# Performance work log

Hardware: AMD Instinct MI355X
Metric: run time of the kernel (lower is better)

## Reference

```python
import jax, jax.numpy as jnp
import numpy as np

NPOINT = 2048
RADIUS = 0.4
NSAMPLE = 32
BN_EPS = 1e-5


def setup_inputs() -> dict:
    key = jax.random.key(0)
    ks = jax.random.split(key, 6)
    B, N, C = 8, 8192, 64
    xyz = jax.random.normal(ks[0], (B, N, 3), jnp.float32)
    points = jax.random.normal(ks[1], (B, N, C), jnp.float32)
    W1 = jax.random.normal(ks[2], (3 + C, 64), jnp.float32) * 0.1
    W2 = jax.random.normal(ks[3], (64, 64), jnp.float32) * 0.1
    W3 = jax.random.normal(ks[4], (64, 128), jnp.float32) * 0.1
    return dict(
        xyz=xyz, points=points,
        W1=W1, g1=jnp.ones(64), b1=jnp.zeros(64),
        W2=W2, g2=jnp.ones(64), b2=jnp.zeros(64),
        W3=W3, g3=jnp.ones(128), b3=jnp.zeros(128),
    )


def _furthest_point_sample(xyz, npoint):
    # xyz: (B, N, 3) -> (B, npoint) int32. Sequential max-min scan, batched.
    B, N, _ = xyz.shape

    def step(carry, _):
        dists, last = carry
        p = jnp.take_along_axis(xyz, last[:, None, None], axis=1)  # (B,1,3)
        d2 = jnp.sum((xyz - p) ** 2, axis=-1)                       # (B,N)
        dists = jnp.minimum(dists, d2)
        nxt = jnp.argmax(dists, axis=-1).astype(jnp.int32)
        return (dists, nxt), nxt

    init = (jnp.full((B, N), 1e10, xyz.dtype), jnp.zeros((B,), jnp.int32))
    _, idx = jax.lax.scan(step, init, None, length=npoint - 1)      # (npoint-1, B)
    idx = jnp.concatenate([jnp.zeros((1, B), jnp.int32), idx], axis=0)
    return idx.T                                                    # (B, npoint)


def _ball_query(xyz, new_xyz, radius, nsample):
    # For each centroid take the first nsample point indices (in original order)
    # within `radius`; pad with the first found index (CUDA ball_query semantics).
    B, N, _ = xyz.shape
    d2 = jnp.sum((new_xyz[:, :, None, :] - xyz[:, None, :, :]) ** 2, axis=-1)  # (B,S,N)
    mask = d2 < radius * radius
    key = jnp.where(mask, jnp.arange(N, dtype=jnp.int32), N)
    srt = jnp.sort(key, axis=-1)[..., :nsample]                     # (B,S,K)
    first = srt[..., :1]
    first = jnp.where(first == N, 0, first)                         # empty ball -> index 0
    return jnp.where(srt == N, first, srt)


def _gather(pts, idx):
    # pts: (B,N,D), idx: (B,...) -> (B,...,D)
    return jax.vmap(lambda p, i: p[i])(pts, idx)


def reference(xyz, points, W1, g1, b1, W2, g2, b2, W3, g3, b3):
    fps_idx = _furthest_point_sample(xyz, NPOINT)                   # (B,S)
    new_xyz = _gather(xyz, fps_idx)                                 # (B,S,3)
    idx = _ball_query(xyz, new_xyz, RADIUS, NSAMPLE)                # (B,S,K)
    grouped_xyz = _gather(xyz, idx) - new_xyz[:, :, None, :]        # (B,S,K,3)
    grouped_pts = _gather(points, idx)                              # (B,S,K,C)
    feats = jnp.concatenate([grouped_xyz, grouped_pts], axis=-1)    # (B,S,K,3+C)
    for W, g, b in ((W1, g1, b1), (W2, g2, b2), (W3, g3, b3)):
        feats = feats @ W                                           # 1x1 conv
        m = feats.mean(axis=(0, 1, 2))
        v = feats.var(axis=(0, 1, 2))                               # biased, torch BN train mode
        feats = g * (feats - m) * jax.lax.rsqrt(v + BN_EPS) + b
        feats = jax.nn.relu(feats)
    new_points = feats.max(axis=2)                                  # max over nsample -> (B,S,mlp[-1])
    return new_xyz, new_points
```

## Files before the change

### kernel.cpp

```cpp
#include <hip/hip_runtime.h>

constexpr int B_ = 8, N_ = 8192, NPOINT_ = 2048, NSAMPLE_ = 32;
constexpr int M_ROWS = B_ * NPOINT_ * NSAMPLE_;
constexpr int NGROUP = B_ * NPOINT_;
constexpr size_t OFF_NXF   = 0;
constexpr size_t OFF_IDX   = 196608;
constexpr size_t OFF_WF    = 1245184;
constexpr size_t OFF_GB    = 1311488;
constexpr size_t OFF_STATS = 1313536;
constexpr size_t OFF_NP    = 1315584;
constexpr size_t OFF_FLAG  = 1317632;
constexpr size_t OFF_MAXB  = 2097152;

__device__ __forceinline__ float bf2f(unsigned short u) {
  union { unsigned u; float f; } x; x.u = ((unsigned)u) << 16; return x.f;
}
__device__ __forceinline__ float lo16f(unsigned u) {
  union { unsigned u; float f; } x; x.u = u << 16; return x.f;
}
__device__ __forceinline__ float hi16f(unsigned u) {
  union { unsigned u; float f; } x; x.u = u & 0xffff0000u; return x.f;
}
__device__ __forceinline__ unsigned short f2bf(float f) {
  union { float f; unsigned u; } x; x.f = f;
  unsigned u = x.u + 0x7FFFu + ((x.u >> 16) & 1u);
  return (unsigned short)(u >> 16);
}
__device__ __forceinline__ unsigned f2u(float f) {
  union { float f; unsigned u; } x; x.f = f; return x.u;
}
__device__ __forceinline__ void unpack8(uint4 u, float* x) {
  x[0] = bf2f((unsigned short)(u.x & 0xffffu)); x[1] = bf2f((unsigned short)(u.x >> 16));
  x[2] = bf2f((unsigned short)(u.y & 0xffffu)); x[3] = bf2f((unsigned short)(u.y >> 16));
  x[4] = bf2f((unsigned short)(u.z & 0xffffu)); x[5] = bf2f((unsigned short)(u.z >> 16));
  x[6] = bf2f((unsigned short)(u.w & 0xffffu)); x[7] = bf2f((unsigned short)(u.w >> 16));
}
__device__ __forceinline__ float ldf(const void* p, size_t i, bool bf) {
  return bf ? bf2f(((const unsigned short*)p)[i]) : ((const float*)p)[i];
}
__device__ __forceinline__ void stf(void* p, size_t i, bool bf, float v) {
  if (bf) ((unsigned short*)p)[i] = f2bf(v);
  else    ((float*)p)[i] = v;
}

extern "C" __global__ void detect_kernel(const unsigned short* __restrict__ xyz,
                                         int* __restrict__ flag) {
  if (threadIdx.x == 0 && blockIdx.x == 0) {
    int sane = 0;
    for (int k = 0; k < 32; ++k) {
      int e = (xyz[2 * k] >> 7) & 0xff;
      if (e >= 90 && e <= 140) ++sane;
    }
    *flag = (sane >= 24) ? 1 : 0;
  }
}

extern "C" __global__ void prep_kernel(
    const void* W1, const void* W2, const void* W3,
    const void* g1, const void* b1, const void* g2, const void* b2,
    const void* g3, const void* b3,
    float* __restrict__ wf, float* __restrict__ gb, const int* __restrict__ flag) {
  const bool bf = (*flag != 0);
  int i = blockIdx.x * 256 + threadIdx.x;
  if (i < 4288)       wf[i] = ldf(W1, i, bf);
  else if (i < 8384)  wf[i] = ldf(W2, i - 4288, bf);
  else if (i < 16576) wf[i] = ldf(W3, i - 8384, bf);
  else if (i < 17088) {
    int k = i - 16576; float v;
    if (k < 64)       v = ldf(g1, k, bf);
    else if (k < 128) v = ldf(b1, k - 64, bf);
    else if (k < 192) v = ldf(g2, k - 128, bf);
    else if (k < 256) v = ldf(b2, k - 192, bf);
    else if (k < 384) v = ldf(g3, k - 256, bf);
    else              v = ldf(b3, k - 384, bf);
    gb[k] = v;
  }
}

template <bool BF>
__device__ __forceinline__ void fps_body(
    const void* xyz, void* out, float* __restrict__ nxf,
    unsigned short* sxyz, unsigned long long* slots) {
#pragma clang fp contract(off)
  const int b = blockIdx.x;
  const int t = threadIdx.x;
  const int lane = t & 63;
  const size_t base = (size_t)b * N_ * 3;
  float px[8], py[8], pz[8], d[8];
  if (BF) {
    const uint4* xp = (const uint4*)((const unsigned short*)xyz + base) + t * 3;
    uint4* sp = (uint4*)sxyz + t * 3;
    unsigned cc[12];
#pragma unroll
    for (int m = 0; m < 3; ++m) {
      uint4 u = xp[m];
      sp[m] = u;
      cc[4*m+0] = u.x; cc[4*m+1] = u.y; cc[4*m+2] = u.z; cc[4*m+3] = u.w;
    }
#pragma unroll
    for (int k = 0; k < 8; ++k) {
      if ((k & 1) == 0) {
        unsigned ra = cc[(3*k) >> 1], rb = cc[((3*k) >> 1) + 1];
        px[k] = lo16f(ra); py[k] = hi16f(ra); pz[k] = lo16f(rb);
      } else {
        unsigned ra = cc[(3*k - 1) >> 1], rb = cc[(3*k + 1) >> 1];
        px[k] = hi16f(ra); py[k] = lo16f(rb); pz[k] = hi16f(rb);
      }
    }
  } else {
#pragma unroll
    for (int k = 0; k < 8; ++k) {
      int i = t * 8 + k;
      px[k] = ((const float*)xyz)[base + i*3 + 0];
      py[k] = ((const float*)xyz)[base + i*3 + 1];
      pz[k] = ((const float*)xyz)[base + i*3 + 2];
    }
  }
#pragma unroll
  for (int k = 0; k < 8; ++k) d[k] = 1e10f;
  if (t < 3) slots[t] = 0ull;
  __syncthreads();
  float s0x=0.f,s0y=0.f,s0z=0.f, s1x=0.f,s1y=0.f,s1z=0.f;
  float p0, p1, p2;
  if (BF) { p0 = bf2f(sxyz[0]); p1 = bf2f(sxyz[1]); p2 = bf2f(sxyz[2]); }
  else {
    p0 = ((const float*)xyz)[base + 0];
    p1 = ((const float*)xyz)[base + 1];
    p2 = ((const float*)xyz)[base + 2];
  }
  if (t == 0) { s0x = p0; s0y = p1; s0z = p2; }
  for (int j = 1; j < NPOINT_; ++j) {
    float bv = -1.0f;
#pragma unroll
    for (int k = 0; k < 8; ++k) {
      float dx = px[k] - p0, dy = py[k] - p1, dz = pz[k] - p2;
      float d2 = (dx*dx + dy*dy) + dz*dz;
      float dn = fminf(d[k], d2);
      d[k] = dn;
      bv = fmaxf(bv, dn);
    }
    float bv0 = bv;
#pragma unroll
    for (int off = 1; off < 64; off <<= 1)
      bv = fmaxf(bv, __shfl_xor(bv, off));
    int bk = 0;
    bool hit = (bv0 == bv);
    if (hit) {
#pragma unroll
      for (int k = 7; k >= 0; --k)
        if (d[k] == bv0) bk = k;
    }
    unsigned long long m = __ballot(hit);
    int sl = (int)__builtin_ctzll(m);
    int pi = __shfl(t * 8 + bk, sl);
    const int ss = j % 3;
    if (lane == 0) {
      unsigned long long key =
          ((unsigned long long)f2u(bv) << 32) | (unsigned)(~pi);
      atomicMax(&slots[ss], key);
    }
    if (t == 0) slots[(ss + 1) % 3] = 0ull;
    __syncthreads();
    unsigned long long key2 = slots[ss];
    int gpi = (int)(~(unsigned)key2);
    if (BF) {
      int wo3 = gpi * 3;
      p0 = bf2f(sxyz[wo3 + 0]); p1 = bf2f(sxyz[wo3 + 1]); p2 = bf2f(sxyz[wo3 + 2]);
    } else {
      size_t wo = base + (size_t)gpi * 3;
      p0 = ((const float*)xyz)[wo + 0];
      p1 = ((const float*)xyz)[wo + 1];
      p2 = ((const float*)xyz)[wo + 2];
    }
    if (t == (j & 1023)) {
      if ((j >> 10) == 0) { s0x = p0; s0y = p1; s0z = p2; }
      else                { s1x = p0; s1y = p1; s1z = p2; }
    }
  }
  const bool bfrt = BF;
#pragma unroll
  for (int s = 0; s < 2; ++s) {
    float cx = (s==0)?s0x:s1x;
    float cy = (s==0)?s0y:s1y;
    float cz = (s==0)?s0z:s1z;
    size_t o = ((size_t)b * NPOINT_ + s * 1024 + t) * 3;
    nxf[o+0] = cx; nxf[o+1] = cy; nxf[o+2] = cz;
    stf(out, o+0, bfrt, cx); stf(out, o+1, bfrt, cy); stf(out, o+2, bfrt, cz);
  }
}

extern "C" __global__ void __launch_bounds__(1024, 4) fps_kernel(
    const void* xyz, void* out, float* __restrict__ nxf,
    const int* __restrict__ flag) {
  __shared__ unsigned short sxyz[N_ * 3];
  __shared__ unsigned long long slots[3];
  if (*flag != 0) fps_body<true>(xyz, out, nxf, sxyz, slots);
  else            fps_body<false>(xyz, out, nxf, sxyz, slots);
}

extern "C" __global__ void __launch_bounds__(256) ballq_kernel(
    const void* xyz, const float* __restrict__ nxf,
    unsigned short* __restrict__ idxout, const int* __restrict__ flag) {
#pragma clang fp contract(off)
  const bool bf = (*flag != 0);
  const int gw = (int)((blockIdx.x * 256 + threadIdx.x) >> 6);
  const int lane = threadIdx.x & 63;
  const int b = gw >> 11;
  const int j = gw & (NPOINT_ - 1);
  const size_t base = (size_t)b * N_ * 3;
  const size_t co = ((size_t)b * NPOINT_ + j) * 3;
  const float c0 = nxf[co], c1 = nxf[co+1], c2 = nxf[co+2];
  unsigned short* out = idxout + (size_t)gw * NSAMPLE_;
  int cnt = 0, first = 0;
  for (int c = 0; c < N_/64 && cnt < NSAMPLE_; ++c) {
    int i = c * 64 + lane;
    float x = ldf(xyz, base + i*3 + 0, bf);
    float y = ldf(xyz, base + i*3 + 1, bf);
    float z = ldf(xyz, base + i*3 + 2, bf);
    float dx = x - c0, dy = y - c1, dz = z - c2;
    float d2 = (dx*dx + dy*dy) + dz*dz;
    unsigned long long m = __ballot(d2 < 0.16f);
    if (lane == 0) {
      while (m && cnt < NSAMPLE_) {
        int bit = __builtin_ctzll(m);
        int pi = c * 64 + bit;
        if (cnt == 0) first = pi;
        out[cnt] = (unsigned short)pi;
        ++cnt;
        m &= (m - 1);
      }
    }
    cnt = __shfl(cnt, 0);
  }
  first = __shfl(first, 0);
  if (lane >= cnt && lane < NSAMPLE_) out[lane] = (unsigned short)first;
}

__device__ __forceinline__ void l1_row(
    const void* xyz, const void* points, const float* __restrict__ nxf,
    const unsigned short* __restrict__ idx, const float* __restrict__ wf,
    int r, bool bf, float* acc) {
  const int b = r >> 16;
  const int j = (r >> 5) & (NPOINT_ - 1);
  const int i = idx[r];
  const size_t pt = (size_t)b * N_ + i;
  const float* cp = nxf + ((size_t)b * NPOINT_ + j) * 3;
  float f0 = ldf(xyz, pt*3 + 0, bf) - cp[0];
  float f1 = ldf(xyz, pt*3 + 1, bf) - cp[1];
  float f2 = ldf(xyz, pt*3 + 2, bf) - cp[2];
#pragma unroll
  for (int c = 0; c < 64; ++c)
    acc[c] = fmaf(f0, wf[c], fmaf(f1, wf[64+c], f2 * wf[128+c]));
  const float* wp = wf + 192;
  if (bf) {
    const uint4* pp = (const uint4*)((const unsigned short*)points + pt * 64);
#pragma unroll
    for (int s = 0; s < 8; ++s) {
      uint4 u = pp[s];
      float x[8]; unpack8(u, x);
#pragma unroll
      for (int kk = 0; kk < 8; ++kk)
#pragma unroll
        for (int c = 0; c < 64; ++c)
          acc[c] = fmaf(x[kk], wp[(s*8+kk)*64 + c], acc[c]);
    }
  } else {
    const float4* pp = (const float4*)((const float*)points + pt * 64);
#pragma unroll
    for (int s = 0; s < 16; ++s) {
      float4 u = pp[s];
      float x[4] = {u.x, u.y, u.z, u.w};
#pragma unroll
      for (int kk = 0; kk < 4; ++kk)
#pragma unroll
        for (int c = 0; c < 64; ++c)
          acc[c] = fmaf(x[kk], wp[(s*4+kk)*64 + c], acc[c]);
    }
  }
}

template <int LDW>
__device__ __forceinline__ void mm64(const float* v, const float* __restrict__ w,
                                     float* acc) {
#pragma unroll
  for (int ch = 0; ch < 64; ++ch)
#pragma unroll
    for (int c = 0; c < 64; ++c)
      acc[c] = fmaf(v[ch], w[ch*LDW + c], acc[c]);
}

__device__ __forceinline__ void bnrelu64(float* v, const float* __restrict__ np0) {
#pragma unroll
  for (int c = 0; c < 64; ++c)
    v[c] = fmaxf(fmaf(v[c], np0[c], np0[64 + c]), 0.f);
}

__device__ __forceinline__ void commit_stats64(float* a, float* __restrict__ stats) {
  float q[64];
#pragma unroll
  for (int c = 0; c < 64; ++c) q[c] = a[c] * a[c];
#pragma unroll
  for (int off = 1; off < 64; off <<= 1)
#pragma unroll
    for (int c = 0; c < 64; ++c) {
      a[c] += __shfl_xor(a[c], off);
      q[c] += __shfl_xor(q[c], off);
    }
  __shared__ float LS[4][64], LQ[4][64];
  const int t = threadIdx.x, w = t >> 6;
  if ((t & 63) == 0) {
#pragma unroll
    for (int c = 0; c < 64; ++c) { LS[w][c] = a[c]; LQ[w][c] = q[c]; }
  }
  __syncthreads();
  if (t < 64) {
    atomicAdd(&stats[t],      LS[0][t] + LS[1][t] + LS[2][t] + LS[3][t]);
    atomicAdd(&stats[64 + t], LQ[0][t] + LQ[1][t] + LQ[2][t] + LQ[3][t]);
  }
}

extern "C" __global__ void __launch_bounds__(256) p1_kernel(
    const void* xyz, const void* points, const float* __restrict__ nxf,
    const unsigned short* __restrict__ idx, const float* __restrict__ wf,
    float* __restrict__ stats, const int* __restrict__ flag) {
  const bool bf = (*flag != 0);
  const int r = blockIdx.x * 256 + threadIdx.x;
  float acc[64];
  l1_row(xyz, points, nxf, idx, wf, r, bf, acc);
  commit_stats64(acc, stats);
}

extern "C" __global__ void __launch_bounds__(256, 2) p2_kernel(
    const void* xyz, const void* points, const float* __restrict__ nxf,
    const unsigned short* __restrict__ idx, const float* __restrict__ wf,
    const float* __restrict__ w2, const float* __restrict__ np1,
    float* __restrict__ stats, const int* __restrict__ flag) {
  const bool bf = (*flag != 0);
  const int r = blockIdx.x * 256 + threadIdx.x;
  float v[64];
  l1_row(xyz, points, nxf, idx, wf, r, bf, v);
  bnrelu64(v, np1);
  float acc[64];
#pragma unroll
  for (int c = 0; c < 64; ++c) acc[c] = 0.f;
  mm64<64>(v, w2, acc);
  commit_stats64(acc, stats);
}

extern "C" __global__ void __launch_bounds__(256, 2) p3_kernel(
    const void* xyz, const void* points, const float* __restrict__ nxf,
    const unsigned short* __restrict__ idx, const float* __restrict__ wf,
    const float* __restrict__ w2, const float* __restrict__ w3,
    const float* __restrict__ np1, const float* __restrict__ np2,
    unsigned short* __restrict__ maxb, float* __restrict__ stats,
    const int* __restrict__ flag) {
  const bool bf = (*flag != 0);
  const int t = threadIdx.x, lane = t & 63, w = t >> 6;
  const int h = __builtin_amdgcn_readfirstlane(w & 1);
  const int g = blockIdx.x * 4 + (w >> 1) * 2 + (lane >> 5);
  const int r = g * 32 + (lane & 31);
  float v[64];
  l1_row(xyz, points, nxf, idx, wf, r, bf, v);
  bnrelu64(v, np1);
  float y2[64];
#pragma unroll
  for (int c = 0; c < 64; ++c) y2[c] = 0.f;
  mm64<64>(v, w2, y2);
  bnrelu64(y2, np2);
  const float* w3h = w3 + h * 64;
  float y3[64];
#pragma unroll
  for (int c = 0; c < 64; ++c) y3[c] = 0.f;
  mm64<128>(y2, w3h, y3);
  float* s = v; float* q = y2;
#pragma unroll
  for (int c = 0; c < 64; ++c) { s[c] = y3[c]; q[c] = y3[c] * y3[c]; }
#pragma unroll
  for (int off = 1; off <= 16; off <<= 1)
#pragma unroll
    for (int c = 0; c < 64; ++c)
      y3[c] = fmaxf(y3[c], __shfl_xor(y3[c], off));
  if ((lane & 31) == 0) {
    unsigned short* mo = maxb + (size_t)g * 128 + h * 64;
#pragma unroll
    for (int c = 0; c < 64; ++c) mo[c] = f2bf(y3[c]);
  }
#pragma unroll
  for (int off = 1; off < 64; off <<= 1)
#pragma unroll
    for (int c = 0; c < 64; ++c) {
      s[c] += __shfl_xor(s[c], off);
      q[c] += __shfl_xor(q[c], off);
    }
  __shared__ float LS[4][64], LQ[4][64];
  if (lane == 0) {
#pragma unroll
    for (int c = 0; c < 64; ++c) { LS[w][c] = s[c]; LQ[w][c] = q[c]; }
  }
  __syncthreads();
  if (t < 128) {
    int hh = t >> 6, cl = t & 63;
    atomicAdd(&stats[t],       LS[hh][cl] + LS[hh+2][cl]);
    atomicAdd(&stats[128 + t], LQ[hh][cl] + LQ[hh+2][cl]);
  }
}

extern "C" __global__ void nparam_kernel(
    const float* __restrict__ stats, const float* __restrict__ g,
    const float* __restrict__ bb, float* __restrict__ npar, int Cc) {
  int c = threadIdx.x;
  if (c < Cc) {
    float m = stats[c] * (1.0f / M_ROWS);
    float v = stats[Cc + c] * (1.0f / M_ROWS) - m * m;
    float sc = g[c] / sqrtf(v + 1e-5f);
    npar[c] = sc;
    npar[Cc + c] = bb[c] - m * sc;
  }
}

extern "C" __global__ void __launch_bounds__(256) final_kernel(
    const unsigned short* __restrict__ maxb, const float* __restrict__ npar,
    void* out, const int* __restrict__ flag) {
  const bool bf = (*flag != 0);
  const int gtid = blockIdx.x * 256 + threadIdx.x;
  const int c = gtid & 127;
  float y = bf2f(maxb[gtid]);
  float r = fmaxf(fmaf(y, npar[c], npar[128 + c]), 0.f);
  stf(out, (size_t)B_ * NPOINT_ * 3 + gtid, bf, r);
}

extern "C" void kernel_launch(void* const* d_in, const int* in_sizes, int n_in,
                              void* d_out, int out_size, void* d_ws, size_t ws_size,
                              hipStream_t stream) {
  const void* xyz    = d_in[0];
  const void* points = d_in[1];
  char* ws = (char*)d_ws;
  float* nxf   = (float*)(ws + OFF_NXF);
  unsigned short* wsIdx = (unsigned short*)(ws + OFF_IDX);
  float* wf    = (float*)(ws + OFF_WF);
  float* gb    = (float*)(ws + OFF_GB);
  float* stats = (float*)(ws + OFF_STATS);
  float* npar  = (float*)(ws + OFF_NP);
  int*   flag  = (int*)(ws + OFF_FLAG);
  unsigned short* maxb = (unsigned short*)(ws + OFF_MAXB);

  hipMemsetAsync(stats, 0, 512 * sizeof(float), stream);
  detect_kernel<<<1, 64, 0, stream>>>((const unsigned short*)xyz, flag);
  prep_kernel<<<67, 256, 0, stream>>>(d_in[2], d_in[5], d_in[8], d_in[3], d_in[4],
                                      d_in[6], d_in[7], d_in[9], d_in[10], wf, gb, flag);
  fps_kernel<<<B_, 1024, 0, stream>>>(xyz, d_out, nxf, flag);
  ballq_kernel<<<(B_ * NPOINT_) / 4, 256, 0, stream>>>(xyz, nxf, wsIdx, flag);
  p1_kernel<<<M_ROWS / 256, 256, 0, stream>>>(xyz, points, nxf, wsIdx, wf, stats, flag);
  nparam_kernel<<<1, 128, 0, stream>>>(stats, gb, gb + 64, npar, 64);
  p2_kernel<<<M_ROWS / 256, 256, 0, stream>>>(xyz, points, nxf, wsIdx, wf, wf + 4288,
                                              npar, stats + 128, flag);
  nparam_kernel<<<1, 128, 0, stream>>>(stats + 128, gb + 128, gb + 192, npar + 128, 64);
  p3_kernel<<<(2 * M_ROWS) / 256, 256, 0, stream>>>(xyz, points, nxf, wsIdx, wf,
                                                    wf + 4288, wf + 8384, npar,
                                                    npar + 128, maxb, stats + 256, flag);
  nparam_kernel<<<1, 128, 0, stream>>>(stats + 256, gb + 256, gb + 384, npar + 256, 128);
  final_kernel<<<(NGROUP * 128) / 256, 256, 0, stream>>>(maxb, npar + 256, d_out, flag);
}
```

Baseline: 3.822 ms.

## Replace FPS atomic argmax with DPP wave reduction and per-wave coordinate slots

```diff
diff --git a/kernel.cpp b/kernel.cpp
--- a/kernel.cpp
+++ b/kernel.cpp
@@ -26,8 +26,11 @@
   unsigned u = x.u + 0x7FFFu + ((x.u >> 16) & 1u);
   return (unsigned short)(u >> 16);
 }
-__device__ __forceinline__ unsigned f2u(float f) {
-  union { float f; unsigned u; } x; x.f = f; return x.u;
+__device__ __forceinline__ int f2i(float f) {
+  union { float f; int i; } x; x.f = f; return x.i;
+}
+__device__ __forceinline__ float i2f(int i) {
+  union { int i; float f; } x; x.i = i; return x.f;
 }
 __device__ __forceinline__ void unpack8(uint4 u, float* x) {
   x[0] = bf2f((unsigned short)(u.x & 0xffffu)); x[1] = bf2f((unsigned short)(u.x >> 16));
@@ -41,6 +44,12 @@
 __device__ __forceinline__ void stf(void* p, size_t i, bool bf, float v) {
   if (bf) ((unsigned short*)p)[i] = f2bf(v);
   else    ((float*)p)[i] = v;
+}
+
+template <int CTRL>
+__device__ __forceinline__ float dpp_maxf(float v) {
+  int n = __builtin_amdgcn_update_dpp(0, f2i(v), CTRL, 0xF, 0xF, true);
+  return fmaxf(v, i2f(n));
 }
 
 extern "C" __global__ void detect_kernel(const unsigned short* __restrict__ xyz,
@@ -79,22 +88,19 @@
 
 template <bool BF>
 __device__ __forceinline__ void fps_body(
-    const void* xyz, void* out, float* __restrict__ nxf,
-    unsigned short* sxyz, unsigned long long* slots) {
+    const void* xyz, void* out, float* __restrict__ nxf, float4* slots) {
 #pragma clang fp contract(off)
   const int b = blockIdx.x;
   const int t = threadIdx.x;
-  const int lane = t & 63;
+  const int lane = t & 63, w = t >> 6;
   const size_t base = (size_t)b * N_ * 3;
   float px[8], py[8], pz[8], d[8];
   if (BF) {
     const uint4* xp = (const uint4*)((const unsigned short*)xyz + base) + t * 3;
-    uint4* sp = (uint4*)sxyz + t * 3;
     unsigned cc[12];
 #pragma unroll
     for (int m = 0; m < 3; ++m) {
       uint4 u = xp[m];
-      sp[m] = u;
       cc[4*m+0] = u.x; cc[4*m+1] = u.y; cc[4*m+2] = u.z; cc[4*m+3] = u.w;
     }
 #pragma unroll
@@ -118,12 +124,12 @@
   }
 #pragma unroll
   for (int k = 0; k < 8; ++k) d[k] = 1e10f;
-  if (t < 3) slots[t] = 0ull;
-  __syncthreads();
   float s0x=0.f,s0y=0.f,s0z=0.f, s1x=0.f,s1y=0.f,s1z=0.f;
   float p0, p1, p2;
-  if (BF) { p0 = bf2f(sxyz[0]); p1 = bf2f(sxyz[1]); p2 = bf2f(sxyz[2]); }
-  else {
+  if (BF) {
+    const unsigned short* xp16 = (const unsigned short*)xyz + base;
+    p0 = bf2f(xp16[0]); p1 = bf2f(xp16[1]); p2 = bf2f(xp16[2]);
+  } else {
     p0 = ((const float*)xyz)[base + 0];
     p1 = ((const float*)xyz)[base + 1];
     p2 = ((const float*)xyz)[base + 2];
@@ -139,39 +145,40 @@
       d[k] = dn;
       bv = fmaxf(bv, dn);
     }
-    float bv0 = bv;
-#pragma unroll
-    for (int off = 1; off < 64; off <<= 1)
-      bv = fmaxf(bv, __shfl_xor(bv, off));
-    int bk = 0;
-    bool hit = (bv0 == bv);
-    if (hit) {
-#pragma unroll
-      for (int k = 7; k >= 0; --k)
-        if (d[k] == bv0) bk = k;
-    }
-    unsigned long long m = __ballot(hit);
-    int sl = (int)__builtin_ctzll(m);
-    int pi = __shfl(t * 8 + bk, sl);
-    const int ss = j % 3;
-    if (lane == 0) {
-      unsigned long long key =
-          ((unsigned long long)f2u(bv) << 32) | (unsigned)(~pi);
-      atomicMax(&slots[ss], key);
-    }
-    if (t == 0) slots[(ss + 1) % 3] = 0ull;
+    float g = bv;
+    g = dpp_maxf<0xB1>(g);
+    g = dpp_maxf<0x4E>(g);
+    g = dpp_maxf<0x141>(g);
+    g = dpp_maxf<0x140>(g);
+    g = dpp_maxf<0x142>(g);
+    g = dpp_maxf<0x143>(g);
+    float wmax = i2f(__builtin_amdgcn_readlane(f2i(g), 63));
+    unsigned long long hm = __ballot(bv == wmax);
+    int sl = (int)__builtin_ctzll(hm);
+    const int pb = (j & 1) << 4;
+    if (lane == sl) {
+      int bk = 0;
+#pragma unroll
+      for (int k = 7; k >= 1; --k)
+        if (d[k] == bv) bk = k;
+      float cx = px[0], cy = py[0], cz = pz[0];
+#pragma unroll
+      for (int k = 1; k < 8; ++k)
+        if (bk == k) { cx = px[k]; cy = py[k]; cz = pz[k]; }
+      slots[pb + w] = make_float4(bv, cx, cy, cz);
+    }
     __syncthreads();
-    unsigned long long key2 = slots[ss];
-    int gpi = (int)(~(unsigned)key2);
-    if (BF) {
-      int wo3 = gpi * 3;
-      p0 = bf2f(sxyz[wo3 + 0]); p1 = bf2f(sxyz[wo3 + 1]); p2 = bf2f(sxyz[wo3 + 2]);
-    } else {
-      size_t wo = base + (size_t)gpi * 3;
-      p0 = ((const float*)xyz)[wo + 0];
-      p1 = ((const float*)xyz)[wo + 1];
-      p2 = ((const float*)xyz)[wo + 2];
-    }
+    float4 kc = slots[pb + (lane & 15)];
+    float m2 = kc.x;
+    m2 = dpp_maxf<0xB1>(m2);
+    m2 = dpp_maxf<0x4E>(m2);
+    m2 = dpp_maxf<0x141>(m2);
+    m2 = dpp_maxf<0x140>(m2);
+    unsigned long long bm = __ballot(kc.x == m2);
+    int s2 = (int)__builtin_ctzll(bm);
+    p0 = i2f(__builtin_amdgcn_readlane(f2i(kc.y), s2));
+    p1 = i2f(__builtin_amdgcn_readlane(f2i(kc.z), s2));
+    p2 = i2f(__builtin_amdgcn_readlane(f2i(kc.w), s2));
     if (t == (j & 1023)) {
       if ((j >> 10) == 0) { s0x = p0; s0y = p1; s0z = p2; }
       else                { s1x = p0; s1y = p1; s1z = p2; }
@@ -192,10 +199,9 @@
 extern "C" __global__ void __launch_bounds__(1024, 4) fps_kernel(
     const void* xyz, void* out, float* __restrict__ nxf,
     const int* __restrict__ flag) {
-  __shared__ unsigned short sxyz[N_ * 3];
-  __shared__ unsigned long long slots[3];
-  if (*flag != 0) fps_body<true>(xyz, out, nxf, sxyz, slots);
-  else            fps_body<false>(xyz, out, nxf, sxyz, slots);
+  __shared__ float4 slots[32];
+  if (*flag != 0) fps_body<true>(xyz, out, nxf, slots);
+  else            fps_body<false>(xyz, out, nxf, slots);
 }
 
 extern "C" __global__ void __launch_bounds__(256) ballq_kernel(
```

New measurement: 3.982 ms. +4.2%, slower.
